# Kernel tuning notes

Measured on AMD Instinct MI355X. Metric: run time of the kernel, lower is better.

The kernel has to match this reference:

```python
import jax, jax.numpy as jnp
import numpy as np

X_CH, Y_CH = 3, 31
C = X_CH + Y_CH            # s_channels = m_channels = 34
A = C * (C - 1) // 2       # 561 Givens rotation angles
SMIN, SMAX = 0.001, 1000.0


def setup_inputs() -> dict:
    key = jax.random.key(0)
    k1, k2 = jax.random.split(key)
    x = jax.random.normal(k1, (4, X_CH, 64, 64), dtype=jnp.float32)
    W = jax.random.normal(k2, (C + C + A, X_CH), dtype=jnp.float32) * 0.1
    b = jnp.zeros((C + C + A,), dtype=jnp.float32)
    return {"x": x, "W": W, "b": b}


def _covariance(s, a):
    # s: (B, C, H, W) positive variances; a: (B, A, H, W) rotation angles.
    B, _, H, Wd = s.shape
    cs = jnp.moveaxis(jnp.cos(a), 1, 0)  # (A, B, H, W)
    ss = jnp.moveaxis(jnp.sin(a), 1, 0)  # (A, B, H, W)
    ii, jj = np.triu_indices(C, k=1)      # same (i, j) order as the torch double loop
    ii = jnp.asarray(ii, dtype=jnp.int32)
    jj = jnp.asarray(jj, dtype=jnp.int32)

    # R starts as identity; each Givens rotation rij only mixes columns i and j
    # of R (R <- R @ rij), so we update two columns instead of a full matmul.
    R0 = jnp.broadcast_to(jnp.eye(C, dtype=s.dtype), (B, H, Wd, C, C))

    def step(R, inp):
        c_, s_, i, j = inp
        col_i = R[..., i]                      # (B, H, W, C)
        col_j = R[..., j]
        c_ = c_[..., None]
        s_ = s_[..., None]
        R = R.at[..., i].set(c_ * col_i + s_ * col_j)
        R = R.at[..., j].set(-s_ * col_i + c_ * col_j)
        return R, None

    R, _ = jax.lax.scan(step, R0, (cs, ss, ii, jj))
    sp = jnp.transpose(s, (0, 2, 3, 1))        # (B, H, W, C)
    # S = R^T D R with D = diag(sp): S[k,n] = sum_m R[m,k] * sp[m] * R[m,n]
    S = jnp.einsum('bhwmk,bhwm,bhwmn->bhwkn', R, sp, R)
    D = jnp.zeros((B, H, Wd, C, C), dtype=s.dtype).at[..., jnp.arange(C), jnp.arange(C)].set(sp)
    return S, R, D


def reference(x, W, b):
    # 1x1-conv encoder: (B, 3, H, W) -> (B, 629, H, W)
    w = jnp.einsum('oc,bchw->bohw', W, x) + b[None, :, None, None]
    m = jnp.transpose(w[:, :C], (0, 2, 3, 1))                  # (B, H, W, C) mean
    s = jax.nn.sigmoid(w[:, C:2 * C])
    s = SMIN * (1.0 - s) + SMAX * s                            # (B, C, H, W)
    a = jnp.pi * jnp.tanh(w[:, 2 * C:])                        # (B, A, H, W)
    S, _, _ = _covariance(s, a)
    return m, S, s
```

## Files before the change

kernel.cpp:

```cpp
#include <hip/hip_runtime.h>


#define CCH 34
#define ACH 561
#define HWPIX 4096
#define NPIX 16384
#define PXB 15
#define TPP 17
#define NTHR 256
#define CSPX (141 * 8)
#define VROW 36
#define VPX (17 * VROW * 4)
#define OFF_S 557056
#define OFF_s 19496960
#define LOG2E 1.4426950408889634f

typedef float    f32x2 __attribute__((ext_vector_type(2)));
typedef _Float16 h2    __attribute__((ext_vector_type(2)));

struct PairsT {
    short i[ACH]; short j[ACH];
    constexpr PairsT() : i(), j() {
        int p = 0;
        for (int a = 0; a < CCH - 1; ++a)
            for (int b = a + 1; b < CCH; ++b) { i[p] = (short)a; j[p] = (short)b; ++p; }
    }
};
__device__ constexpr PairsT PR{};

__device__ __forceinline__ float dot2h(h2 a, h2 b, float c) {
#if __has_builtin(__builtin_amdgcn_fdot2)
    return __builtin_amdgcn_fdot2(a, b, c, false);
#else
    return fmaf((float)a[0], (float)b[0], fmaf((float)a[1], (float)b[1], c));
#endif
}

__device__ __forceinline__ void rot2(f32x2& Ri, f32x2& Rj, f32x2 c2, f32x2 s2) {
    f32x2 t1 = s2 * Rj;
    f32x2 t2 = s2 * Ri;
    Ri = __builtin_elementwise_fma(c2, Ri, t1);
    Rj = __builtin_elementwise_fma(c2, Rj, -t2);
}

template <int P0, int P1>
__device__ __forceinline__ void apply_rots(f32x2* R2, const char* csb) {
    #pragma unroll
    for (int k = P0; k < P1; ++k) {
        f32x2 cell = *(const f32x2*)(csb + (k - P0) * 8);
        f32x2 c2 = __builtin_shufflevector(cell, cell, 0, 0);
        f32x2 s2 = __builtin_shufflevector(cell, cell, 1, 1);
        rot2(R2[PR.i[k]], R2[PR.j[k]], c2, s2);
    }
}

__device__ __forceinline__ float2 cs_of(float wv) {
    float e  = __builtin_amdgcn_exp2f((2.0f * LOG2E) * wv);
    float tt = 1.0f - 2.0f * __builtin_amdgcn_rcpf(e + 1.0f);
    float rv = 0.5f * tt;
    return make_float2(__builtin_amdgcn_cosf(rv), __builtin_amdgcn_sinf(rv));
}

template <int G0, int LEN>
__device__ __forceinline__ void fill_cs(const float* __restrict__ Wm,
                                        const float* __restrict__ bvec,
                                        const float* xs, char* csbuf,
                                        int npx, int t) {
    for (int o = t; o < npx * LEN; o += NTHR) {
        int px = (int)((unsigned)o / (unsigned)LEN);
        int l  = o - px * LEN;
        int ch = 2 * CCH + G0 + l;
        float wv = fmaf(Wm[ch*3+0], xs[px*3+0],
                   fmaf(Wm[ch*3+1], xs[px*3+1], Wm[ch*3+2] * xs[px*3+2])) + bvec[ch];
        *(float2*)(csbuf + px * CSPX + l * 8) = cs_of(wv);
    }
}

__global__ __launch_bounds__(NTHR, 4) void gpd_kernel(
    const float* __restrict__ x,
    const float* __restrict__ Wm,
    const float* __restrict__ bvec,
    float* __restrict__ out)
{
    __shared__ alignas(16) char vbuf[PXB * VPX];
    __shared__ _Float16 lds_sh[PXB * CCH];
    __shared__ float xs[PXB * 3];

    const int t   = threadIdx.x;
    const int p0  = blockIdx.x * PXB;
    const int npx = min(PXB, NPIX - p0);

    for (int i = t; i < npx * 3; i += NTHR) {
        int px = (int)((unsigned)i / 3u); int c = i - px * 3;
        int p = p0 + px; int b = p >> 12; int hw = p & 4095;
        xs[i] = x[(b * 3 + c) * HWPIX + hw];
    }
    __syncthreads();

    for (int o = t; o < npx * 68; o += NTHR) {
        int q = (int)((unsigned)o / 68u); int ch = o - q * 68;
        int p = p0 + q; int b = p >> 12; int hw = p & 4095;
        float wv = fmaf(Wm[ch*3+0], xs[q*3+0],
                   fmaf(Wm[ch*3+1], xs[q*3+1], Wm[ch*3+2] * xs[q*3+2])) + bvec[ch];
        if (ch < CCH) {
            out[(size_t)p * CCH + ch] = wv;
        } else {
            float e  = __builtin_amdgcn_exp2f(-wv * LOG2E);
            float sg = __builtin_amdgcn_rcpf(1.0f + e);
            float sv = fmaf(999.999f, sg, 0.001f);
            int c = ch - CCH;
            out[OFF_s + (size_t)(b * CCH + c) * HWPIX + hw] = sv;
            lds_sh[q * CCH + c] = (_Float16)sv;
        }
    }

    const int px = t / TPP;
    const int u  = t - px * TPP;
    const bool act = (px < npx) && (px < PXB);
    const char* csb = vbuf + px * CSPX;

    f32x2 R2[CCH];
    #pragma unroll
    for (int n = 0; n < CCH; ++n) {
        R2[n][0] = (n == 2 * u)     ? 1.0f : 0.0f;
        R2[n][1] = (n == 2 * u + 1) ? 1.0f : 0.0f;
    }

    fill_cs<0, 141>(Wm, bvec, xs, vbuf, npx, t);
    __syncthreads();
    if (act) apply_rots<0, 141>(R2, csb);
    __syncthreads();
    fill_cs<141, 140>(Wm, bvec, xs, vbuf, npx, t);
    __syncthreads();
    if (act) apply_rots<141, 281>(R2, csb);
    __syncthreads();
    fill_cs<281, 140>(Wm, bvec, xs, vbuf, npx, t);
    __syncthreads();
    if (act) apply_rots<281, 421>(R2, csb);
    __syncthreads();
    fill_cs<421, 140>(Wm, bvec, xs, vbuf, npx, t);
    __syncthreads();
    if (act) apply_rots<421, 561>(R2, csb);
    __syncthreads();

    if (act) {
        unsigned* vb = (unsigned*)(vbuf + px * VPX) + u * VROW;
        #pragma unroll
        for (int n = 0; n < CCH; ++n)
            vb[n] = __builtin_bit_cast(unsigned,
                        __builtin_amdgcn_cvt_pkrtz(R2[n][0], R2[n][1]));
    }
    __syncthreads();

    if (act) {
        const unsigned* vb = (const unsigned*)(vbuf + px * VPX);
        const _Float16* sh = lds_sh + px * CCH;
        float aL[CCH], aH[CCH];
        #pragma unroll
        for (int n = 0; n < CCH; ++n) { aL[n] = 0.0f; aH[n] = 0.0f; }
        for (int mp = 0; mp < 17; ++mp) {
            const unsigned* row = vb + mp * VROW;
            h2 sh2 = *(const h2*)(sh + 2 * mp);
            h2 vkL = __builtin_bit_cast(h2, row[2 * u])     * sh2;
            h2 vkH = __builtin_bit_cast(h2, row[2 * u + 1]) * sh2;
            #pragma unroll
            for (int g = 0; g < 8; ++g) {
                uint4 rr = *(const uint4*)(row + 4 * g);
                h2 r0 = __builtin_bit_cast(h2, rr.x), r1 = __builtin_bit_cast(h2, rr.y);
                h2 r2 = __builtin_bit_cast(h2, rr.z), r3 = __builtin_bit_cast(h2, rr.w);
                aL[4*g+0] = dot2h(vkL, r0, aL[4*g+0]);  aH[4*g+0] = dot2h(vkH, r0, aH[4*g+0]);
                aL[4*g+1] = dot2h(vkL, r1, aL[4*g+1]);  aH[4*g+1] = dot2h(vkH, r1, aH[4*g+1]);
                aL[4*g+2] = dot2h(vkL, r2, aL[4*g+2]);  aH[4*g+2] = dot2h(vkH, r2, aH[4*g+2]);
                aL[4*g+3] = dot2h(vkL, r3, aL[4*g+3]);  aH[4*g+3] = dot2h(vkH, r3, aH[4*g+3]);
            }
            uint2 rr2 = *(const uint2*)(row + 32);
            h2 r32 = __builtin_bit_cast(h2, rr2.x), r33 = __builtin_bit_cast(h2, rr2.y);
            aL[32] = dot2h(vkL, r32, aL[32]);  aH[32] = dot2h(vkH, r32, aH[32]);
            aL[33] = dot2h(vkL, r33, aL[33]);  aH[33] = dot2h(vkH, r33, aH[33]);
        }
        float* os = out + OFF_S + (size_t)(p0 + px) * (CCH * CCH) + 2 * u * CCH;
        #pragma unroll
        for (int q = 0; q < 17; ++q) {
            float4 v;
            v.x = (4*q+0 < 34) ? aL[4*q+0] : aH[4*q+0-34];
            v.y = (4*q+1 < 34) ? aL[4*q+1] : aH[4*q+1-34];
            v.z = (4*q+2 < 34) ? aL[4*q+2] : aH[4*q+2-34];
            v.w = (4*q+3 < 34) ? aL[4*q+3] : aH[4*q+3-34];
            *(float4*)(os + 4 * q) = v;
        }
    }
}

extern "C" void kernel_launch(void* const* d_in, const int* in_sizes, int n_in,
                              void* d_out, int out_size, void* d_ws, size_t ws_size,
                              hipStream_t stream) {
    const float* x  = (const float*)d_in[0];
    const float* W  = (const float*)d_in[1];
    const float* bv = (const float*)d_in[2];
    float* out = (float*)d_out;
    const int nblk = (NPIX + PXB - 1) / PXB;
    hipLaunchKernelGGL(gpd_kernel, dim3(nblk), dim3(NTHR), 0, stream,
                       x, W, bv, out);
}
```

Measured before the change: 81.16 us.

## Halve block size and stage rotation rows in two LDS passes

Shrinks each block to 7 pixels with 128 threads and splits the R^T D R accumulation into two passes over half of the rotation rows. Each pass stages only 9 or 8 rows in LDS, so the LDS buffer is roughly halved and more blocks can be resident per CU. The cost is two extra barriers, fp16 packed rows held in registers across the passes (more register pressure), and more blocks with a ragged tail.

New measurement: 78.66 us. 3.1% less time.

```diff
diff --git a/kernel.cpp b/kernel.cpp
--- a/kernel.cpp
+++ b/kernel.cpp
@@ -5,12 +5,12 @@
 #define ACH 561
 #define HWPIX 4096
 #define NPIX 16384
-#define PXB 15
+#define PXB 7
 #define TPP 17
-#define NTHR 256
+#define NTHR 128
 #define CSPX (141 * 8)
 #define VROW 36
-#define VPX (17 * VROW * 4)
+#define VHPX (9 * VROW * 4)
 #define OFF_S 557056
 #define OFF_s 19496960
 #define LOG2E 1.4426950408889634f
@@ -76,13 +76,38 @@
     }
 }
 
+template <int GOFF, int NMP>
+__device__ __forceinline__ void accum_pass(const unsigned* vb, const _Float16* sh,
+                                           int u, float* aL, float* aH) {
+    for (int mp = 0; mp < NMP; ++mp) {
+        const unsigned* row = vb + mp * VROW;
+        h2 sh2 = *(const h2*)(sh + 2 * (GOFF + mp));
+        h2 vkL = __builtin_bit_cast(h2, row[2 * u])     * sh2;
+        h2 vkH = __builtin_bit_cast(h2, row[2 * u + 1]) * sh2;
+        #pragma unroll
+        for (int g = 0; g < 8; ++g) {
+            uint4 rr = *(const uint4*)(row + 4 * g);
+            h2 r0 = __builtin_bit_cast(h2, rr.x), r1 = __builtin_bit_cast(h2, rr.y);
+            h2 r2 = __builtin_bit_cast(h2, rr.z), r3 = __builtin_bit_cast(h2, rr.w);
+            aL[4*g+0] = dot2h(vkL, r0, aL[4*g+0]);  aH[4*g+0] = dot2h(vkH, r0, aH[4*g+0]);
+            aL[4*g+1] = dot2h(vkL, r1, aL[4*g+1]);  aH[4*g+1] = dot2h(vkH, r1, aH[4*g+1]);
+            aL[4*g+2] = dot2h(vkL, r2, aL[4*g+2]);  aH[4*g+2] = dot2h(vkH, r2, aH[4*g+2]);
+            aL[4*g+3] = dot2h(vkL, r3, aL[4*g+3]);  aH[4*g+3] = dot2h(vkH, r3, aH[4*g+3]);
+        }
+        uint2 rr2 = *(const uint2*)(row + 32);
+        h2 r32 = __builtin_bit_cast(h2, rr2.x), r33 = __builtin_bit_cast(h2, rr2.y);
+        aL[32] = dot2h(vkL, r32, aL[32]);  aH[32] = dot2h(vkH, r32, aH[32]);
+        aL[33] = dot2h(vkL, r33, aL[33]);  aH[33] = dot2h(vkH, r33, aH[33]);
+    }
+}
+
 __global__ __launch_bounds__(NTHR, 4) void gpd_kernel(
     const float* __restrict__ x,
     const float* __restrict__ Wm,
     const float* __restrict__ bvec,
     float* __restrict__ out)
 {
-    __shared__ alignas(16) char vbuf[PXB * VPX];
+    __shared__ alignas(16) char vbuf[PXB * VHPX];
     __shared__ _Float16 lds_sh[PXB * CCH];
     __shared__ float xs[PXB * 3];
 
@@ -143,41 +168,36 @@
     if (act) apply_rots<421, 561>(R2, csb);
     __syncthreads();
 
+    unsigned rh[CCH];
+    #pragma unroll
+    for (int n = 0; n < CCH; ++n)
+        rh[n] = __builtin_bit_cast(unsigned,
+                    __builtin_amdgcn_cvt_pkrtz(R2[n][0], R2[n][1]));
+
+    unsigned* vreg = (unsigned*)(vbuf + px * VHPX);
+    const _Float16* sh = lds_sh + px * CCH;
+    float aL[CCH], aH[CCH];
+    #pragma unroll
+    for (int n = 0; n < CCH; ++n) { aL[n] = 0.0f; aH[n] = 0.0f; }
+
+    if (act && u < 9) {
+        unsigned* dst = vreg + u * VROW;
+        #pragma unroll
+        for (int n = 0; n < CCH; ++n) dst[n] = rh[n];
+    }
+    __syncthreads();
+    if (act) accum_pass<0, 9>(vreg, sh, u, aL, aH);
+    __syncthreads();
+
+    if (act && u >= 9) {
+        unsigned* dst = vreg + (u - 9) * VROW;
+        #pragma unroll
+        for (int n = 0; n < CCH; ++n) dst[n] = rh[n];
+    }
+    __syncthreads();
     if (act) {
-        unsigned* vb = (unsigned*)(vbuf + px * VPX) + u * VROW;
-        #pragma unroll
-        for (int n = 0; n < CCH; ++n)
-            vb[n] = __builtin_bit_cast(unsigned,
-                        __builtin_amdgcn_cvt_pkrtz(R2[n][0], R2[n][1]));
-    }
-    __syncthreads();
-
-    if (act) {
-        const unsigned* vb = (const unsigned*)(vbuf + px * VPX);
-        const _Float16* sh = lds_sh + px * CCH;
-        float aL[CCH], aH[CCH];
-        #pragma unroll
-        for (int n = 0; n < CCH; ++n) { aL[n] = 0.0f; aH[n] = 0.0f; }
-        for (int mp = 0; mp < 17; ++mp) {
-            const unsigned* row = vb + mp * VROW;
-            h2 sh2 = *(const h2*)(sh + 2 * mp);
-            h2 vkL = __builtin_bit_cast(h2, row[2 * u])     * sh2;
-            h2 vkH = __builtin_bit_cast(h2, row[2 * u + 1]) * sh2;
-            #pragma unroll
-            for (int g = 0; g < 8; ++g) {
-                uint4 rr = *(const uint4*)(row + 4 * g);
-                h2 r0 = __builtin_bit_cast(h2, rr.x), r1 = __builtin_bit_cast(h2, rr.y);
-                h2 r2 = __builtin_bit_cast(h2, rr.z), r3 = __builtin_bit_cast(h2, rr.w);
-                aL[4*g+0] = dot2h(vkL, r0, aL[4*g+0]);  aH[4*g+0] = dot2h(vkH, r0, aH[4*g+0]);
-                aL[4*g+1] = dot2h(vkL, r1, aL[4*g+1]);  aH[4*g+1] = dot2h(vkH, r1, aH[4*g+1]);
-                aL[4*g+2] = dot2h(vkL, r2, aL[4*g+2]);  aH[4*g+2] = dot2h(vkH, r2, aH[4*g+2]);
-                aL[4*g+3] = dot2h(vkL, r3, aL[4*g+3]);  aH[4*g+3] = dot2h(vkH, r3, aH[4*g+3]);
-            }
-            uint2 rr2 = *(const uint2*)(row + 32);
-            h2 r32 = __builtin_bit_cast(h2, rr2.x), r33 = __builtin_bit_cast(h2, rr2.y);
-            aL[32] = dot2h(vkL, r32, aL[32]);  aH[32] = dot2h(vkH, r32, aH[32]);
-            aL[33] = dot2h(vkL, r33, aL[33]);  aH[33] = dot2h(vkH, r33, aH[33]);
-        }
+        accum_pass<9, 8>(vreg, sh, u, aL, aH);
+
         float* os = out + OFF_S + (size_t)(p0 + px) * (CCH * CCH) + 2 * u * CCH;
         #pragma unroll
         for (int q = 0; q < 17; ++q) {
```
